# Optimization experiments

Hardware: AMD Instinct MI355X
Metric: run time of the kernel (lower is better)

The kernel has to match this reference:

```python
import jax, jax.numpy as jnp
import numpy as np

BETA = 0.25


def setup_inputs() -> dict:
    key = jax.random.key(0)
    k1, k2 = jax.random.split(key)
    latents = jax.random.normal(k1, (16, 32, 32, 256), dtype=jnp.float32)
    codebook = jax.random.normal(k2, (8192, 256), dtype=jnp.float32) * 0.05
    return {"latents": latents, "codebook": codebook}


def reference(latents, codebook):
    # latents: [B, H, W, D]; codebook: [V, D]
    B, H, W, D = latents.shape
    flat = latents.reshape(-1, D)  # [N, D], N = B*H*W
    dist = (jnp.sum(flat * flat, axis=1, keepdims=True)
            + jnp.sum(codebook * codebook, axis=1)
            - 2.0 * jnp.einsum('nd,vd->nv', flat, codebook))  # [N, V]
    min_encoding_indices = jnp.argmin(dist, axis=1)  # [N]
    quantized = codebook[min_encoding_indices].reshape(B, H, W, D)
    sg = jax.lax.stop_gradient
    codebook_loss = (jnp.mean((sg(quantized) - latents) ** 2)
                     + BETA * jnp.mean((quantized - sg(latents)) ** 2))
    # straight-through estimator
    quantized_st = latents + sg(quantized - latents)
    return quantized_st, codebook_loss, min_encoding_indices
```

## Files before the change

### kernel.cpp

```cpp
#include <hip/hip_runtime.h>

#define N_ROWS 16384
#define DDIM   256
#define VCODES 8192
#define BETA   0.25f

using f16   = _Float16;
using f16x4 = __attribute__((ext_vector_type(4))) _Float16;
using f16x8 = __attribute__((ext_vector_type(8))) _Float16;
using f32x4 = __attribute__((ext_vector_type(4))) float;

typedef __attribute__((address_space(1))) const unsigned int gu32_t;
typedef __attribute__((address_space(3))) unsigned int       lu32_t;

__device__ __forceinline__ void gload16(const void* g, void* l) {
    __builtin_amdgcn_global_load_lds((gu32_t*)g, (lu32_t*)l, 16, 0, 0);
}


__global__ void split_lat(const float* __restrict__ lat, f16* __restrict__ Ap) {
    int t = blockIdx.x * 256 + threadIdx.x;
    float4 x = *(const float4*)&lat[(size_t)t * 4];
    int row = t >> 6;
    int c   = (t & 63) * 4;
    f16 h0 = (f16)x.x, h1 = (f16)x.y, h2 = (f16)x.z, h3 = (f16)x.w;
    f16 l0 = (f16)(x.x - (float)h0), l1 = (f16)(x.y - (float)h1);
    f16 l2 = (f16)(x.z - (float)h2), l3 = (f16)(x.w - (float)h3);
    f16x4 hi = {h0, h1, h2, h3}, lo = {l0, l1, l2, l3};
    int kt  = c >> 5;
    int sub = ((c & 31) >> 3) * 128 + (row & 15) * 8 + (c & 7);
    size_t base = ((size_t)(row >> 4) * 16);
    *(f16x4*)&Ap[(base + kt)     * 512 + sub] = hi;
    *(f16x4*)&Ap[(base + kt + 8) * 512 + sub] = lo;
}

__global__ void split_cb(const float* __restrict__ cb, f16* __restrict__ Bp) {
    int t = blockIdx.x * 256 + threadIdx.x;
    float4 e = *(const float4*)&cb[(size_t)t * 4];
    float ex = e.x * 64.0f, ey = e.y * 64.0f, ez = e.z * 64.0f, ew = e.w * 64.0f;
    int row = t >> 6;
    int c   = (t & 63) * 4;
    f16 h0 = (f16)ex, h1 = (f16)ey, h2 = (f16)ez, h3 = (f16)ew;
    f16 l0 = (f16)(ex - (float)h0), l1 = (f16)(ey - (float)h1);
    f16 l2 = (f16)(ez - (float)h2), l3 = (f16)(ew - (float)h3);
    f16x4 hi = {h0, h1, h2, h3}, lo = {l0, l1, l2, l3};
    int kt  = c >> 5;
    int sub = ((c & 31) >> 3) * 128 + (row & 15) * 8 + (c & 7);
    size_t base = ((size_t)(row >> 4) * 16);
    *(f16x4*)&Bp[(base + kt)     * 512 + sub] = hi;
    *(f16x4*)&Bp[(base + kt + 8) * 512 + sub] = lo;
}

__global__ void cbnorm_k(const float* __restrict__ cb, float* __restrict__ cbnorm) {
    int gtid = blockIdx.x * blockDim.x + threadIdx.x;
    int wave = gtid >> 6;
    int lane = threadIdx.x & 63;
    if (wave >= VCODES) return;
    float4 v = *(const float4*)(cb + (size_t)wave * DDIM + lane * 4);
    float s = v.x * v.x + v.y * v.y + v.z * v.z + v.w * v.w;
    #pragma unroll
    for (int m = 32; m; m >>= 1) s += __shfl_xor(s, m, 64);
    if (lane == 0) cbnorm[wave] = s;
}

__global__ __launch_bounds__(512, 2)
void vq_mfma(const f16* __restrict__ Ap, const f16* __restrict__ Bp,
             const float* __restrict__ cbn,
             float* __restrict__ pmin, int* __restrict__ pidx) {
    __shared__ __align__(16) f16 L[2][16384];

    const int tid  = threadIdx.x;
    const int lane = tid & 63;
    const int w    = tid >> 6;
    const int wr   = w >> 2;
    const int wc   = w & 3;
    const int l15  = lane & 15;
    const int l4   = lane >> 4;

    const int id  = blockIdx.x;
    const int swz = (id & 7) * 256 + (id >> 3);
    const int bx  = swz & 63;
    const int by  = swz >> 6;

    const char* Ag = (const char*)Ap + (size_t)bx * 262144;
    const char* Bg = (const char*)Bp + (size_t)by * 262144;

    auto stage = [&](int vk, int b) {
        const int akt = (vk < 8) ? vk : vk - 8;
        const int bkt = (vk < 16) ? vk : vk - 16;
        #pragma unroll
        for (int i = 0; i < 2; i++) {
            const int off = i * 8192 + tid * 16;
            const int s   = off >> 10;
            const int win = off & 1023;
            gload16(Ag + (size_t)(s * 16 + akt) * 1024 + win, (char*)&L[b][0] + off);
        }
        #pragma unroll
        for (int i = 0; i < 2; i++) {
            const int off = i * 8192 + tid * 16;
            const int s   = off >> 10;
            const int win = off & 1023;
            gload16(Bg + (size_t)(s * 16 + bkt) * 1024 + win, (char*)&L[b][0] + 16384 + off);
        }
    };

    f32x4 acc[8][4];
    #pragma unroll
    for (int m = 0; m < 8; m++)
        #pragma unroll
        for (int n = 0; n < 4; n++) acc[m][n] = (f32x4){0.f, 0.f, 0.f, 0.f};

    stage(0, 0);
    int cur = 0;

    for (int vk = 0; vk < 24; vk++) {
        __syncthreads();
        if (vk < 23) stage(vk + 1, cur ^ 1);

        const f16* Abase = &L[cur][0]    + (wr * 8) * 512;
        const f16* Bbase = &L[cur][8192] + (wc * 4) * 512;

        f16x8 bf[4], af[8];
        #pragma unroll
        for (int n = 0; n < 4; n++) bf[n] = *(const f16x8*)(Bbase + n * 512 + lane * 8);
        #pragma unroll
        for (int mm = 0; mm < 8; mm++) af[mm] = *(const f16x8*)(Abase + mm * 512 + lane * 8);

        __builtin_amdgcn_s_setprio(1);
        #pragma unroll
        for (int mm = 0; mm < 8; mm++)
            #pragma unroll
            for (int n = 0; n < 4; n++)
                acc[mm][n] = __builtin_amdgcn_mfma_f32_16x16x32_f16(af[mm], bf[n], acc[mm][n], 0, 0, 0);
        __builtin_amdgcn_s_setprio(0);

        cur ^= 1;
    }

    float* sMin = (float*)&L[0][0];
    int*   sIdx = (int*)((char*)&L[0][0] + 4096);

    #pragma unroll
    for (int m = 0; m < 8; m++) {
        float rmin[4]; int ridx[4];
        #pragma unroll
        for (int r = 0; r < 4; r++) { rmin[r] = 3.4e38f; ridx[r] = 0x7fffffff; }
        #pragma unroll
        for (int n = 0; n < 4; n++) {
            const int c = by * 256 + wc * 64 + n * 16 + l15;
            const float cn = cbn[c];
            #pragma unroll
            for (int r = 0; r < 4; r++) {
                float s = cn - acc[m][n][r] * 0.03125f;
                if (s < rmin[r] || (s == rmin[r] && c < ridx[r])) { rmin[r] = s; ridx[r] = c; }
            }
        }
        #pragma unroll
        for (int r = 0; r < 4; r++) {
            float mv = rmin[r]; int idv = ridx[r];
            #pragma unroll
            for (int o = 1; o < 16; o <<= 1) {
                float om = __shfl_xor(mv, o, 64);
                int  oid = __shfl_xor(idv, o, 64);
                if (om < mv || (om == mv && oid < idv)) { mv = om; idv = oid; }
            }
            if (l15 == 0) {
                const int rloc = wr * 128 + m * 16 + l4 * 4 + r;
                sMin[wc * 256 + rloc] = mv;
                sIdx[wc * 256 + rloc] = idv;
            }
        }
    }
    __syncthreads();

    if (tid < 256) {
        float mv = sMin[tid]; int idv = sIdx[tid];
        #pragma unroll
        for (int j = 1; j < 4; j++) {
            float om = sMin[j * 256 + tid]; int oid = sIdx[j * 256 + tid];
            if (om < mv || (om == mv && oid < idv)) { mv = om; idv = oid; }
        }
        pmin[(bx * 256 + tid) * 32 + by] = mv;
        pidx[(bx * 256 + tid) * 32 + by] = idv;
    }
}

__global__ void combine_k(const float* __restrict__ lat, const float* __restrict__ cb,
                          const float* __restrict__ pmin, const int* __restrict__ pidx,
                          float* __restrict__ out_q, float* __restrict__ out_idx,
                          float* __restrict__ loss_part) {
    const int tid = threadIdx.x, lane = tid & 63, wv = tid >> 6;
    const int row = blockIdx.x * 4 + wv;

    float m = 3.4e38f; int id = 0x7fffffff;
    if (lane < 32) { m = pmin[row * 32 + lane]; id = pidx[row * 32 + lane]; }
    #pragma unroll
    for (int o = 32; o; o >>= 1) {
        float om = __shfl_xor(m, o, 64);
        int  oid = __shfl_xor(id, o, 64);
        if (om < m || (om == m && oid < id)) { m = om; id = oid; }
    }

    float4 q = *(const float4*)&cb[(size_t)id * DDIM + lane * 4];
    float4 x = *(const float4*)&lat[(size_t)row * DDIM + lane * 4];
    *(float4*)&out_q[(size_t)row * DDIM + lane * 4] = q;
    if (lane == 0) out_idx[row] = (float)id;

    float dx = q.x - x.x, dy = q.y - x.y, dz = q.z - x.z, dw = q.w - x.w;
    float s = dx * dx + dy * dy + dz * dz + dw * dw;
    #pragma unroll
    for (int o = 32; o; o >>= 1) s += __shfl_xor(s, o, 64);

    __shared__ float red[4];
    if (lane == 0) red[wv] = s;
    __syncthreads();
    if (tid == 0) loss_part[blockIdx.x] = red[0] + red[1] + red[2] + red[3];
}

__global__ void loss_k(const float* __restrict__ part, float* __restrict__ out_loss) {
    float s = 0.0f;
    for (int i = threadIdx.x; i < N_ROWS / 4; i += 256) s += part[i];
    #pragma unroll
    for (int m = 32; m; m >>= 1) s += __shfl_xor(s, m, 64);
    __shared__ float wsum[4];
    int lane = threadIdx.x & 63, w = threadIdx.x >> 6;
    if (lane == 0) wsum[w] = s;
    __syncthreads();
    if (threadIdx.x == 0) {
        float t = wsum[0] + wsum[1] + wsum[2] + wsum[3];
        *out_loss = (1.0f + BETA) * t / (float)((size_t)N_ROWS * DDIM);
    }
}

extern "C" void kernel_launch(void* const* d_in, const int* in_sizes, int n_in,
                              void* d_out, int out_size, void* d_ws, size_t ws_size,
                              hipStream_t stream) {
    const float* lat = (const float*)d_in[0];
    const float* cb  = (const float*)d_in[1];

    float* ws = (float*)d_ws;
    f16*   Ap       = (f16*)ws;
    f16*   Bp       = (f16*)(ws + 4194304);
    float* cbn      = ws + 4194304 + 2097152;
    float* pmin     = cbn + VCODES;
    int*   pidx     = (int*)(pmin + N_ROWS * 32);
    float* losspart = (float*)(pidx + N_ROWS * 32);

    float* out_q    = (float*)d_out;
    float* out_loss = out_q + (size_t)N_ROWS * DDIM;
    float* out_idx  = out_loss + 1;

    split_lat<<<N_ROWS * DDIM / 1024, 256, 0, stream>>>(lat, Ap);
    split_cb<<<VCODES * DDIM / 1024, 256, 0, stream>>>(cb, Bp);
    cbnorm_k<<<VCODES / 4, 256, 0, stream>>>(cb, cbn);

    vq_mfma<<<2048, 512, 0, stream>>>(Ap, Bp, cbn, pmin, pidx);

    combine_k<<<N_ROWS / 4, 256, 0, stream>>>(lat, cb, pmin, pidx,
                                              out_q, out_idx, losspart);
    loss_k<<<1, 256, 0, stream>>>(losspart, out_loss);
}
```

Measured before the change: 322.8 us.

## Deepen LDS pipeline to four stages with split A/B prefetch and explicit waitcnt

Replaces the double-buffered K loop with a four-buffer ring that prefetches three K-steps ahead. A and B tile loads are issued separately, interleaved between two half-steps of MFMA work, and synchronised with manual vmcnt/lgkmcnt waits and raw barriers instead of __syncthreads. The goal is to hide global-to-LDS latency more fully. The cost is doubling LDS to 128KB per block, which likely allows only one block per CU, plus extra barriers per iteration.

```diff
diff --git a/kernel.cpp b/kernel.cpp
--- a/kernel.cpp
+++ b/kernel.cpp
@@ -67,7 +67,7 @@
 void vq_mfma(const f16* __restrict__ Ap, const f16* __restrict__ Bp,
              const float* __restrict__ cbn,
              float* __restrict__ pmin, int* __restrict__ pidx) {
-    __shared__ __align__(16) f16 L[2][16384];
+    __shared__ __align__(16) f16 L[4][16384];
 
     const int tid  = threadIdx.x;
     const int lane = tid & 63;
@@ -85,9 +85,8 @@
     const char* Ag = (const char*)Ap + (size_t)bx * 262144;
     const char* Bg = (const char*)Bp + (size_t)by * 262144;
 
-    auto stage = [&](int vk, int b) {
+    auto stageA = [&](int vk, int b) {
         const int akt = (vk < 8) ? vk : vk - 8;
-        const int bkt = (vk < 16) ? vk : vk - 16;
         #pragma unroll
         for (int i = 0; i < 2; i++) {
             const int off = i * 8192 + tid * 16;
@@ -95,6 +94,9 @@
             const int win = off & 1023;
             gload16(Ag + (size_t)(s * 16 + akt) * 1024 + win, (char*)&L[b][0] + off);
         }
+    };
+    auto stageB = [&](int vk, int b) {
+        const int bkt = (vk < 16) ? vk : vk - 16;
         #pragma unroll
         for (int i = 0; i < 2; i++) {
             const int off = i * 8192 + tid * 16;
@@ -110,31 +112,51 @@
         #pragma unroll
         for (int n = 0; n < 4; n++) acc[m][n] = (f32x4){0.f, 0.f, 0.f, 0.f};
 
-    stage(0, 0);
-    int cur = 0;
+    stageA(0, 0); stageB(0, 0);
+    stageA(1, 1); stageB(1, 1);
+    stageA(2, 2); stageB(2, 2);
+    asm volatile("s_waitcnt vmcnt(8)" ::: "memory");
+    __builtin_amdgcn_s_barrier();
 
     for (int vk = 0; vk < 24; vk++) {
-        __syncthreads();
-        if (vk < 23) stage(vk + 1, cur ^ 1);
-
-        const f16* Abase = &L[cur][0]    + (wr * 8) * 512;
-        const f16* Bbase = &L[cur][8192] + (wc * 4) * 512;
-
-        f16x8 bf[4], af[8];
+        const int b = vk & 3;
+        const f16* Abase = &L[b][0]    + (wr * 8) * 512;
+        const f16* Bbase = &L[b][8192] + (wc * 4) * 512;
+
+        f16x8 bf[4], af[4];
         #pragma unroll
         for (int n = 0; n < 4; n++) bf[n] = *(const f16x8*)(Bbase + n * 512 + lane * 8);
         #pragma unroll
-        for (int mm = 0; mm < 8; mm++) af[mm] = *(const f16x8*)(Abase + mm * 512 + lane * 8);
-
+        for (int mm = 0; mm < 4; mm++) af[mm] = *(const f16x8*)(Abase + mm * 512 + lane * 8);
+        if (vk < 21) stageA(vk + 3, (vk + 3) & 3);
+        __builtin_amdgcn_s_barrier();
+        asm volatile("s_waitcnt lgkmcnt(0)" ::: "memory");
         __builtin_amdgcn_s_setprio(1);
         #pragma unroll
-        for (int mm = 0; mm < 8; mm++)
+        for (int mm = 0; mm < 4; mm++)
             #pragma unroll
             for (int n = 0; n < 4; n++)
                 acc[mm][n] = __builtin_amdgcn_mfma_f32_16x16x32_f16(af[mm], bf[n], acc[mm][n], 0, 0, 0);
         __builtin_amdgcn_s_setprio(0);
-
-        cur ^= 1;
+        __builtin_amdgcn_s_barrier();
+
+        f16x8 af2[4];
+        #pragma unroll
+        for (int mm = 0; mm < 4; mm++) af2[mm] = *(const f16x8*)(Abase + (4 + mm) * 512 + lane * 8);
+        if (vk < 21) stageB(vk + 3, (vk + 3) & 3);
+        if (vk <= 20)      { asm volatile("s_waitcnt vmcnt(8)" ::: "memory"); }
+        else if (vk == 21) { asm volatile("s_waitcnt vmcnt(4)" ::: "memory"); }
+        else if (vk == 22) { asm volatile("s_waitcnt vmcnt(0)" ::: "memory"); }
+        __builtin_amdgcn_s_barrier();
+        asm volatile("s_waitcnt lgkmcnt(0)" ::: "memory");
+        __builtin_amdgcn_s_setprio(1);
+        #pragma unroll
+        for (int mm = 0; mm < 4; mm++)
+            #pragma unroll
+            for (int n = 0; n < 4; n++)
+                acc[4 + mm][n] = __builtin_amdgcn_mfma_f32_16x16x32_f16(af2[mm], bf[n], acc[4 + mm][n], 0, 0, 0);
+        __builtin_amdgcn_s_setprio(0);
+        __builtin_amdgcn_s_barrier();
     }
 
     float* sMin = (float*)&L[0][0];
```

After: 349.6 us. 8.3% more time.

## Use single fp16 GEMM pass with top-2 candidates and fp32 rescoring

Applied to the files above, without the earlier changes.

Replaces the three-term split-fp16 distance GEMM (hi*hi, hi*lo, lo*hi over 24 k-steps) with one plain fp16 GEMM over 8 k-steps. The argmin is kept exact by tracking the top-2 candidates per 256-code tile, then rescoring in full fp32 in the combine kernel every candidate within a fixed margin of the global minimum. This cuts the matrix-core work and operand traffic to about a third. In exchange the combine kernel gets more work, partial-result buffers double in size, and correctness relies on the fp16 error staying below the margin and on the true winner being in some tile's top two.

```diff
diff --git a/kernel.cpp b/kernel.cpp
--- a/kernel.cpp
+++ b/kernel.cpp
@@ -4,6 +4,7 @@
 #define DDIM   256
 #define VCODES 8192
 #define BETA   0.25f
+#define DELTA  0.02f
 
 using f16   = _Float16;
 using f16x4 = __attribute__((ext_vector_type(4))) _Float16;
@@ -23,32 +24,24 @@
     float4 x = *(const float4*)&lat[(size_t)t * 4];
     int row = t >> 6;
     int c   = (t & 63) * 4;
-    f16 h0 = (f16)x.x, h1 = (f16)x.y, h2 = (f16)x.z, h3 = (f16)x.w;
-    f16 l0 = (f16)(x.x - (float)h0), l1 = (f16)(x.y - (float)h1);
-    f16 l2 = (f16)(x.z - (float)h2), l3 = (f16)(x.w - (float)h3);
-    f16x4 hi = {h0, h1, h2, h3}, lo = {l0, l1, l2, l3};
+    f16x4 hi = {(f16)x.x, (f16)x.y, (f16)x.z, (f16)x.w};
     int kt  = c >> 5;
     int sub = ((c & 31) >> 3) * 128 + (row & 15) * 8 + (c & 7);
-    size_t base = ((size_t)(row >> 4) * 16);
-    *(f16x4*)&Ap[(base + kt)     * 512 + sub] = hi;
-    *(f16x4*)&Ap[(base + kt + 8) * 512 + sub] = lo;
+    size_t base = ((size_t)(row >> 4) * 8);
+    *(f16x4*)&Ap[(base + kt) * 512 + sub] = hi;
 }
 
 __global__ void split_cb(const float* __restrict__ cb, f16* __restrict__ Bp) {
     int t = blockIdx.x * 256 + threadIdx.x;
     float4 e = *(const float4*)&cb[(size_t)t * 4];
-    float ex = e.x * 64.0f, ey = e.y * 64.0f, ez = e.z * 64.0f, ew = e.w * 64.0f;
+    f16x4 hi = {(f16)(e.x * 64.0f), (f16)(e.y * 64.0f),
+                (f16)(e.z * 64.0f), (f16)(e.w * 64.0f)};
     int row = t >> 6;
     int c   = (t & 63) * 4;
-    f16 h0 = (f16)ex, h1 = (f16)ey, h2 = (f16)ez, h3 = (f16)ew;
-    f16 l0 = (f16)(ex - (float)h0), l1 = (f16)(ey - (float)h1);
-    f16 l2 = (f16)(ez - (float)h2), l3 = (f16)(ew - (float)h3);
-    f16x4 hi = {h0, h1, h2, h3}, lo = {l0, l1, l2, l3};
     int kt  = c >> 5;
     int sub = ((c & 31) >> 3) * 128 + (row & 15) * 8 + (c & 7);
-    size_t base = ((size_t)(row >> 4) * 16);
-    *(f16x4*)&Bp[(base + kt)     * 512 + sub] = hi;
-    *(f16x4*)&Bp[(base + kt + 8) * 512 + sub] = lo;
+    size_t base = ((size_t)(row >> 4) * 8);
+    *(f16x4*)&Bp[(base + kt) * 512 + sub] = hi;
 }
 
 __global__ void cbnorm_k(const float* __restrict__ cb, float* __restrict__ cbnorm) {
@@ -63,10 +56,16 @@
     if (lane == 0) cbnorm[wave] = s;
 }
 
+__device__ __forceinline__ void ins2(float v, int i,
+                                     float& m1, int& i1, float& m2, int& i2) {
+    if (v < m1 || (v == m1 && i < i1)) { m2 = m1; i2 = i1; m1 = v; i1 = i; }
+    else if (v < m2 || (v == m2 && i < i2)) { m2 = v; i2 = i; }
+}
+
 __global__ __launch_bounds__(512, 2)
 void vq_mfma(const f16* __restrict__ Ap, const f16* __restrict__ Bp,
              const float* __restrict__ cbn,
-             float* __restrict__ pmin, int* __restrict__ pidx) {
+             float* __restrict__ pmin2, int* __restrict__ pidx2) {
     __shared__ __align__(16) f16 L[2][16384];
 
     const int tid  = threadIdx.x;
@@ -82,25 +81,23 @@
     const int bx  = swz & 63;
     const int by  = swz >> 6;
 
-    const char* Ag = (const char*)Ap + (size_t)bx * 262144;
-    const char* Bg = (const char*)Bp + (size_t)by * 262144;
+    const char* Ag = (const char*)Ap + (size_t)bx * 131072;
+    const char* Bg = (const char*)Bp + (size_t)by * 131072;
 
     auto stage = [&](int vk, int b) {
-        const int akt = (vk < 8) ? vk : vk - 8;
-        const int bkt = (vk < 16) ? vk : vk - 16;
         #pragma unroll
         for (int i = 0; i < 2; i++) {
             const int off = i * 8192 + tid * 16;
             const int s   = off >> 10;
             const int win = off & 1023;
-            gload16(Ag + (size_t)(s * 16 + akt) * 1024 + win, (char*)&L[b][0] + off);
+            gload16(Ag + (size_t)(s * 8 + vk) * 1024 + win, (char*)&L[b][0] + off);
         }
         #pragma unroll
         for (int i = 0; i < 2; i++) {
             const int off = i * 8192 + tid * 16;
             const int s   = off >> 10;
             const int win = off & 1023;
-            gload16(Bg + (size_t)(s * 16 + bkt) * 1024 + win, (char*)&L[b][0] + 16384 + off);
+            gload16(Bg + (size_t)(s * 8 + vk) * 1024 + win, (char*)&L[b][0] + 16384 + off);
         }
     };
 
@@ -113,9 +110,9 @@
     stage(0, 0);
     int cur = 0;
 
-    for (int vk = 0; vk < 24; vk++) {
+    for (int vk = 0; vk < 8; vk++) {
         __syncthreads();
-        if (vk < 23) stage(vk + 1, cur ^ 1);
+        if (vk < 7) stage(vk + 1, cur ^ 1);
 
         const f16* Abase = &L[cur][0]    + (wr * 8) * 512;
         const f16* Bbase = &L[cur][8192] + (wc * 4) * 512;
@@ -138,13 +135,13 @@
     }
 
     float* sMin = (float*)&L[0][0];
-    int*   sIdx = (int*)((char*)&L[0][0] + 4096);
+    int*   sIdx = (int*)((char*)&L[0][0] + 8192);
 
     #pragma unroll
     for (int m = 0; m < 8; m++) {
-        float rmin[4]; int ridx[4];
-        #pragma unroll
-        for (int r = 0; r < 4; r++) { rmin[r] = 3.4e38f; ridx[r] = 0x7fffffff; }
+        float m1[4], m2[4]; int i1[4], i2[4];
+        #pragma unroll
+        for (int r = 0; r < 4; r++) { m1[r] = 3.4e38f; m2[r] = 3.4e38f; i1[r] = 0x7fffffff; i2[r] = 0x7fffffff; }
         #pragma unroll
         for (int n = 0; n < 4; n++) {
             const int c = by * 256 + wc * 64 + n * 16 + l15;
@@ -152,59 +149,92 @@
             #pragma unroll
             for (int r = 0; r < 4; r++) {
                 float s = cn - acc[m][n][r] * 0.03125f;
-                if (s < rmin[r] || (s == rmin[r] && c < ridx[r])) { rmin[r] = s; ridx[r] = c; }
+                ins2(s, c, m1[r], i1[r], m2[r], i2[r]);
             }
         }
         #pragma unroll
         for (int r = 0; r < 4; r++) {
-            float mv = rmin[r]; int idv = ridx[r];
+            float a1 = m1[r], a2 = m2[r]; int b1 = i1[r], b2 = i2[r];
             #pragma unroll
             for (int o = 1; o < 16; o <<= 1) {
-                float om = __shfl_xor(mv, o, 64);
-                int  oid = __shfl_xor(idv, o, 64);
-                if (om < mv || (om == mv && oid < idv)) { mv = om; idv = oid; }
+                float oa1 = __shfl_xor(a1, o, 64); int ob1 = __shfl_xor(b1, o, 64);
+                float oa2 = __shfl_xor(a2, o, 64); int ob2 = __shfl_xor(b2, o, 64);
+                if (oa1 < a1 || (oa1 == a1 && ob1 < b1)) {
+                    float nm2; int ni2;
+                    if (a1 < oa2 || (a1 == oa2 && b1 < ob2)) { nm2 = a1; ni2 = b1; }
+                    else                                     { nm2 = oa2; ni2 = ob2; }
+                    a1 = oa1; b1 = ob1; a2 = nm2; b2 = ni2;
+                } else {
+                    if (oa1 < a2 || (oa1 == a2 && ob1 < b2)) { a2 = oa1; b2 = ob1; }
+                }
             }
             if (l15 == 0) {
                 const int rloc = wr * 128 + m * 16 + l4 * 4 + r;
-                sMin[wc * 256 + rloc] = mv;
-                sIdx[wc * 256 + rloc] = idv;
+                sMin[(wc * 256 + rloc) * 2 + 0] = a1;
+                sMin[(wc * 256 + rloc) * 2 + 1] = a2;
+                sIdx[(wc * 256 + rloc) * 2 + 0] = b1;
+                sIdx[(wc * 256 + rloc) * 2 + 1] = b2;
             }
         }
     }
     __syncthreads();
 
     if (tid < 256) {
-        float mv = sMin[tid]; int idv = sIdx[tid];
-        #pragma unroll
-        for (int j = 1; j < 4; j++) {
-            float om = sMin[j * 256 + tid]; int oid = sIdx[j * 256 + tid];
-            if (om < mv || (om == mv && oid < idv)) { mv = om; idv = oid; }
-        }
-        pmin[(bx * 256 + tid) * 32 + by] = mv;
-        pidx[(bx * 256 + tid) * 32 + by] = idv;
+        float m1 = 3.4e38f, m2 = 3.4e38f; int i1 = 0x7fffffff, i2 = 0x7fffffff;
+        #pragma unroll
+        for (int j = 0; j < 4; j++)
+            #pragma unroll
+            for (int k = 0; k < 2; k++) {
+                float v = sMin[(j * 256 + tid) * 2 + k];
+                int   iv = sIdx[(j * 256 + tid) * 2 + k];
+                ins2(v, iv, m1, i1, m2, i2);
+            }
+        const size_t rbase = (size_t)(bx * 256 + tid) * 64 + by * 2;
+        pmin2[rbase + 0] = m1; pmin2[rbase + 1] = m2;
+        pidx2[rbase + 0] = i1; pidx2[rbase + 1] = i2;
     }
 }
 
 __global__ void combine_k(const float* __restrict__ lat, const float* __restrict__ cb,
-                          const float* __restrict__ pmin, const int* __restrict__ pidx,
+                          const float* __restrict__ cbn,
+                          const float* __restrict__ pmin2, const int* __restrict__ pidx2,
                           float* __restrict__ out_q, float* __restrict__ out_idx,
                           float* __restrict__ loss_part) {
     const int tid = threadIdx.x, lane = tid & 63, wv = tid >> 6;
     const int row = blockIdx.x * 4 + wv;
 
-    float m = 3.4e38f; int id = 0x7fffffff;
-    if (lane < 32) { m = pmin[row * 32 + lane]; id = pidx[row * 32 + lane]; }
-    #pragma unroll
-    for (int o = 32; o; o >>= 1) {
-        float om = __shfl_xor(m, o, 64);
-        int  oid = __shfl_xor(id, o, 64);
-        if (om < m || (om == m && oid < id)) { m = om; id = oid; }
-    }
-
-    float4 q = *(const float4*)&cb[(size_t)id * DDIM + lane * 4];
+    float val = pmin2[(size_t)row * 64 + lane];
+    int   idv = pidx2[(size_t)row * 64 + lane];
+
+    float g = val;
+    #pragma unroll
+    for (int o = 32; o; o >>= 1) g = fminf(g, __shfl_xor(g, o, 64));
+
+    unsigned long long mask = __ballot(val <= g + DELTA);
     float4 x = *(const float4*)&lat[(size_t)row * DDIM + lane * 4];
+
+    int idx;
+    if (__popcll(mask) == 1) {
+        idx = __shfl(idv, (int)__builtin_ctzll(mask), 64);
+    } else {
+        float bs = 3.4e38f; int bi = 0x7fffffff;
+        unsigned long long mm = mask;
+        while (mm) {
+            int l = (int)__builtin_ctzll(mm); mm &= mm - 1;
+            int cand = __shfl(idv, l, 64);
+            float4 e = *(const float4*)&cb[(size_t)cand * DDIM + lane * 4];
+            float d = x.x * e.x + x.y * e.y + x.z * e.z + x.w * e.w;
+            #pragma unroll
+            for (int o = 32; o; o >>= 1) d += __shfl_xor(d, o, 64);
+            float s = cbn[cand] - 2.0f * d;
+            if (s < bs || (s == bs && cand < bi)) { bs = s; bi = cand; }
+        }
+        idx = bi;
+    }
+
+    float4 q = *(const float4*)&cb[(size_t)idx * DDIM + lane * 4];
     *(float4*)&out_q[(size_t)row * DDIM + lane * 4] = q;
-    if (lane == 0) out_idx[row] = (float)id;
+    if (lane == 0) out_idx[row] = (float)idx;
 
     float dx = q.x - x.x, dy = q.y - x.y, dz = q.z - x.z, dw = q.w - x.w;
     float s = dx * dx + dy * dy + dz * dz + dw * dw;
@@ -240,11 +270,11 @@
 
     float* ws = (float*)d_ws;
     f16*   Ap       = (f16*)ws;
-    f16*   Bp       = (f16*)(ws + 4194304);
-    float* cbn      = ws + 4194304 + 2097152;
-    float* pmin     = cbn + VCODES;
-    int*   pidx     = (int*)(pmin + N_ROWS * 32);
-    float* losspart = (float*)(pidx + N_ROWS * 32);
+    f16*   Bp       = (f16*)(ws + 2097152);
+    float* cbn      = ws + 2097152 + 1048576;
+    float* pmin2    = cbn + VCODES;
+    int*   pidx2    = (int*)(pmin2 + (size_t)N_ROWS * 64);
+    float* losspart = (float*)(pidx2 + (size_t)N_ROWS * 64);
 
     float* out_q    = (float*)d_out;
     float* out_loss = out_q + (size_t)N_ROWS * DDIM;
@@ -254,9 +284,9 @@
     split_cb<<<VCODES * DDIM / 1024, 256, 0, stream>>>(cb, Bp);
     cbnorm_k<<<VCODES / 4, 256, 0, stream>>>(cb, cbn);
 
-    vq_mfma<<<2048, 512, 0, stream>>>(Ap, Bp, cbn, pmin, pidx);
-
-    combine_k<<<N_ROWS / 4, 256, 0, stream>>>(lat, cb, pmin, pidx,
+    vq_mfma<<<2048, 512, 0, stream>>>(Ap, Bp, cbn, pmin2, pidx2);
+
+    combine_k<<<N_ROWS / 4, 256, 0, stream>>>(lat, cb, cbn, pmin2, pidx2,
                                               out_q, out_idx, losspart);
     loss_k<<<1, 256, 0, stream>>>(losspart, out_loss);
 }
```

Measured after the change: 688.2 us. 113% more time.
